# Kernel tuning notes

Hardware: AMD Instinct MI355X
Metric: run time of the kernel (lower is better)

## Reference

```python
import jax, jax.numpy as jnp
import numpy as np

H = 1024      # hidden_size
I = 512       # intermediate_size
E = 8         # n_routed_experts
TOPK = 2      # num_experts_per_tok
NGROUP = 4    # n_group
TOPKG = 2     # topk_group
SCALE = 1.0   # routed_scaling_factor
B, S = 4, 1024


def setup_inputs() -> dict:
    key = jax.random.key(0)
    k0, k1, k2, k3, k4 = jax.random.split(key, 5)
    return {
        "hidden_states": jax.random.normal(k0, (B, S, H), jnp.float32),
        "gate_weight": jax.random.normal(k1, (E, H), jnp.float32) * (1.0 / np.sqrt(H)),
        "e_score_correction_bias": jnp.zeros((E,), jnp.float32),
        "gate_proj": jax.random.normal(k2, (E, I, H), jnp.float32) * 0.02,
        "up_proj": jax.random.normal(k3, (E, I, H), jnp.float32) * 0.02,
        "down_proj": jax.random.normal(k4, (E, H, I), jnp.float32) * 0.02,
    }


def _gate(xf, gate_weight, bias):
    # xf: [T, H]
    T = xf.shape[0]
    logits = xf @ gate_weight.T                       # [T, E]
    scores = jax.nn.sigmoid(logits)
    scores_for_choice = scores + bias[None, :]
    gsz = E // NGROUP
    # group score: sum of top-2 corrected scores within each group
    grp = scores_for_choice.reshape(T, NGROUP, gsz)
    group_scores = jax.lax.top_k(grp, 2)[0].sum(-1)   # [T, NGROUP]
    _, group_idx = jax.lax.top_k(group_scores, TOPKG)  # [T, TOPKG]
    rows = jnp.arange(T)[:, None]
    group_mask = jnp.zeros((T, NGROUP), xf.dtype).at[rows, group_idx].set(1.0)
    score_mask = jnp.broadcast_to(group_mask[:, :, None], (T, NGROUP, gsz)).reshape(T, E)
    tmp_scores = jnp.where(score_mask > 0, scores_for_choice, 0.0)
    _, topk_idx = jax.lax.top_k(tmp_scores, TOPK)      # [T, TOPK]
    topk_weight = jnp.take_along_axis(scores, topk_idx, axis=1)
    if TOPK > 1:  # norm_topk_prob=True
        topk_weight = topk_weight / (topk_weight.sum(-1, keepdims=True) + 1e-20)
    topk_weight = topk_weight * SCALE
    return topk_idx, topk_weight


def reference(hidden_states, gate_weight, e_score_correction_bias,
              gate_proj, up_proj, down_proj):
    Bv, Sv, Hv = hidden_states.shape
    xf = hidden_states.reshape(-1, Hv).astype(jnp.float32)   # [T, H]
    topk_idx, topk_weight = _gate(xf, gate_weight.astype(jnp.float32),
                                  e_score_correction_bias.astype(jnp.float32))
    # Routed experts: loop over the small fixed expert set; each expert does a
    # dense GEMM over all tokens and results are combined with the (sparse)
    # per-token routing weight. Mathematically identical to the per-pair
    # gather-GEMM kernel, since expert output depends only on (token, expert).
    y = jnp.zeros_like(xf)
    for e in range(E):
        combine_w = jnp.where(topk_idx == e, topk_weight, 0.0).sum(-1)  # [T]
        g = xf @ gate_proj[e].T                                          # [T, I]
        u = xf @ up_proj[e].T                                            # [T, I]
        o = (jax.nn.silu(g) * u) @ down_proj[e].T                        # [T, H]
        y = y + combine_w[:, None] * o
    return y.reshape(Bv, Sv, Hv)
```

## Files before the change

kernel.cpp:

```cpp
#include <hip/hip_runtime.h>
#include <hip/hip_bf16.h>
#include <math.h>

#define H_DIM   1024
#define I_DIM   512
#define NEXP    8
#define NGROUP  4
#define T_TOK   4096
#define NPAIR   8192
#define SCALE   1.0f

typedef float f32x4 __attribute__((ext_vector_type(4)));
typedef short bf16x8 __attribute__((ext_vector_type(8)));
typedef short s16x4 __attribute__((ext_vector_type(4)));
typedef unsigned int u32;

static constexpr size_t OFF_ECNT  = 0;
static constexpr size_t OFF_ELIST = 1024;
static constexpr size_t OFF_EW    = OFF_ELIST + (size_t)NEXP * T_TOK * 4;
static constexpr size_t OFF_SEL   = 512 * 1024;
static constexpr size_t OFF_SELW  = 512 * 1024 + 64 * 1024;
static constexpr size_t MB = 1u << 20;
static constexpr size_t OFF_XH   = 1 * MB;
static constexpr size_t OFF_XL   = 9 * MB;
static constexpr size_t OFF_WGH  = 17 * MB;
static constexpr size_t OFF_WGL  = 25 * MB;
static constexpr size_t OFF_WUH  = 33 * MB;
static constexpr size_t OFF_WUL  = 41 * MB;
static constexpr size_t OFF_WDH  = 49 * MB;
static constexpr size_t OFF_WDL  = 57 * MB;
static constexpr size_t OFF_ACTH = 65 * MB;
static constexpr size_t OFF_ACTL = 73 * MB;
static constexpr size_t WS_NEED  = 81 * MB;
static constexpr size_t OFF_ACT_FB = 1 * MB;

__device__ __forceinline__ void gl_lds16(void* lds, const void* g) {
    __builtin_amdgcn_global_load_lds(
        (const __attribute__((address_space(1))) u32*)g,
        (__attribute__((address_space(3))) u32*)lds, 16, 0, 0);
}

__device__ __forceinline__ void split1(float v, short& h, short& l) {
    const u32 b = __float_as_uint(v);
    h = (short)(b >> 16);
    const float r = v - __uint_as_float(b & 0xffff0000u);
    l = (short)(__float_as_uint(r) >> 16);
}

__device__ __forceinline__ f32x4 mmac3(bf16x8 ah, bf16x8 al, bf16x8 bh,
                                       bf16x8 bl, f32x4 c) {
    c = __builtin_amdgcn_mfma_f32_16x16x32_bf16(ah, bh, c, 0, 0, 0);
    c = __builtin_amdgcn_mfma_f32_16x16x32_bf16(ah, bl, c, 0, 0, 0);
    c = __builtin_amdgcn_mfma_f32_16x16x32_bf16(al, bh, c, 0, 0, 0);
    return c;
}

__device__ __forceinline__ bf16x8 frag16(const short* tile, int row, int boff) {
    return *(const bf16x8*)((const char*)tile + row * 128 + boff);
}

__global__ __launch_bounds__(256)
void cvt_x_gate(const float* __restrict__ x,
                const float* __restrict__ gw,
                const float* __restrict__ bias,
                short* __restrict__ xh, short* __restrict__ xl,
                int* __restrict__ sel, float2* __restrict__ selw) {
    const int t = blockIdx.x;
    const int tid = threadIdx.x;
    const int lane = tid & 63;
    const int wv = tid >> 6;
    const int h = tid * 4;

    const f32x4 xv = *(const f32x4*)(x + (size_t)t * H_DIM + h);
    s16x4 hv, lv;
#pragma unroll
    for (int j = 0; j < 4; ++j) {
        short hh, ll;
        split1(xv[j], hh, ll);
        hv[j] = hh;
        lv[j] = ll;
    }
    *(s16x4*)(xh + (size_t)t * H_DIM + h) = hv;
    *(s16x4*)(xl + (size_t)t * H_DIM + h) = lv;

    float acc[NEXP];
#pragma unroll
    for (int e = 0; e < NEXP; ++e) {
        const f32x4 g = *(const f32x4*)(gw + e * H_DIM + h);
        float a = xv[0] * g[0];
        a = fmaf(xv[1], g[1], a);
        a = fmaf(xv[2], g[2], a);
        a = fmaf(xv[3], g[3], a);
        acc[e] = a;
    }
#pragma unroll
    for (int e = 0; e < NEXP; ++e) {
        float v = acc[e];
#pragma unroll
        for (int s = 32; s > 0; s >>= 1) v += __shfl_xor(v, s, 64);
        acc[e] = v;
    }
    __shared__ float red[4][NEXP];
    if (lane == 0) {
#pragma unroll
        for (int e = 0; e < NEXP; ++e) red[wv][e] = acc[e];
    }
    __syncthreads();
    if (tid == 0) {
        float scores[NEXP], corr[NEXP];
#pragma unroll
        for (int e = 0; e < NEXP; ++e) {
            const float s = red[0][e] + red[1][e] + red[2][e] + red[3][e];
            scores[e] = 1.0f / (1.0f + expf(-s));
            corr[e] = scores[e] + bias[e];
        }
        float gs[NGROUP];
#pragma unroll
        for (int g = 0; g < NGROUP; ++g) gs[g] = corr[2 * g] + corr[2 * g + 1];
        int g0 = 0;
#pragma unroll
        for (int g = 1; g < NGROUP; ++g) if (gs[g] > gs[g0]) g0 = g;
        int g1 = -1;
#pragma unroll
        for (int g = 0; g < NGROUP; ++g) {
            if (g == g0) continue;
            if (g1 < 0 || gs[g] > gs[g1]) g1 = g;
        }
        int e0 = -1;
#pragma unroll
        for (int e = 0; e < NEXP; ++e) {
            const int g = e >> 1;
            if (g != g0 && g != g1) continue;
            if (e0 < 0 || corr[e] > corr[e0]) e0 = e;
        }
        int e1 = -1;
#pragma unroll
        for (int e = 0; e < NEXP; ++e) {
            const int g = e >> 1;
            if ((g != g0 && g != g1) || e == e0) continue;
            if (e1 < 0 || corr[e] > corr[e1]) e1 = e;
        }
        float w0 = scores[e0], w1 = scores[e1];
        const float inv = 1.0f / (w0 + w1 + 1e-20f);
        w0 *= inv * SCALE;
        w1 *= inv * SCALE;
        sel[t] = e0 | (e1 << 8);
        selw[t] = make_float2(w0, w1);
    }
}

__global__ __launch_bounds__(256)
void build_lists(const int* __restrict__ sel, const float2* __restrict__ selw,
                 int* __restrict__ ecnt, int* __restrict__ elist,
                 float* __restrict__ elist_w) {
    const int e = blockIdx.x;
    const int tid = threadIdx.x;
    const int lane = tid & 63;
    const int wv = tid >> 6;
    const int base = tid * (T_TOK / 256);

    int c = 0;
#pragma unroll
    for (int i = 0; i < T_TOK / 256; ++i) {
        const int s = sel[base + i];
        if ((s & 0xff) == e || ((s >> 8) & 0xff) == e) ++c;
    }
    int v = c;
#pragma unroll
    for (int d = 1; d < 64; d <<= 1) {
        const int o = __shfl_up(v, d, 64);
        if (lane >= d) v += o;
    }
    __shared__ int wsum[4];
    if (lane == 63) wsum[wv] = v;
    __syncthreads();
    int waveoff = 0;
#pragma unroll
    for (int w = 0; w < 4; ++w) waveoff += (w < wv) ? wsum[w] : 0;
    int p = waveoff + v - c;
#pragma unroll
    for (int i = 0; i < T_TOK / 256; ++i) {
        const int t = base + i;
        const int s = sel[t];
        const float2 w2 = selw[t];
        if ((s & 0xff) == e) {
            elist[e * T_TOK + p] = t * 2;
            elist_w[e * T_TOK + p] = w2.x;
            ++p;
        } else if (((s >> 8) & 0xff) == e) {
            elist[e * T_TOK + p] = t * 2 + 1;
            elist_w[e * T_TOK + p] = w2.y;
            ++p;
        }
    }
    if (tid == 0) ecnt[e] = wsum[0] + wsum[1] + wsum[2] + wsum[3];
}

__global__ __launch_bounds__(256)
void cvt_w_kernel(const float* __restrict__ src, short* __restrict__ h,
                  short* __restrict__ l, int n) {
    const int i = (blockIdx.x * 256 + threadIdx.x) * 4;
    if (i >= n) return;
    const f32x4 v = *(const f32x4*)(src + i);
    s16x4 hv, lv;
#pragma unroll
    for (int j = 0; j < 4; ++j) {
        short hh, ll;
        split1(v[j], hh, ll);
        hv[j] = hh;
        lv[j] = ll;
    }
    *(s16x4*)(h + i) = hv;
    *(s16x4*)(l + i) = lv;
}

__global__ __launch_bounds__(256)
void gemm1_planar(const short* __restrict__ xh, const short* __restrict__ xl,
                  const short* __restrict__ wgh, const short* __restrict__ wgl,
                  const short* __restrict__ wuh, const short* __restrict__ wul,
                  const int* __restrict__ ecnt, const int* __restrict__ elist,
                  short* __restrict__ acth, short* __restrict__ actl) {
    const int e = blockIdx.z;
    const int cnt = ecnt[e];
    const int row0 = blockIdx.x * 64;
    if (row0 >= cnt) return;
    const int col0 = blockIdx.y * 64;

    __shared__ __align__(16) short xhb[4096], xlb[4096];
    __shared__ __align__(16) short ghb[4096], glb[4096];
    __shared__ __align__(16) short uhb[4096], ulb[4096];

    const int tid = threadIdx.x, lane = tid & 63, wv = tid >> 6;
    const int wr = wv >> 1, wc = wv & 1;
    const int laneR = lane & 15, laneQ = lane >> 4;
    const int* el = elist + e * T_TOK;

    size_t xoff[2], woff[2];
    int ldso[2];
#pragma unroll
    for (int l = 0; l < 2; ++l) {
        const int ci = tid + l * 256;
        const int row = ci >> 3;
        const int c = (ci & 7) ^ (row & 7);
        ldso[l] = ci * 16;
        const int rr = row0 + row;
        const int v = (rr < cnt) ? el[rr] : 0;
        xoff[l] = (size_t)(v >> 1) * H_DIM + c * 8;
        woff[l] = ((size_t)e * I_DIM + col0 + row) * H_DIM + c * 8;
    }

    f32x4 ag[2][2], au[2][2];
#pragma unroll
    for (int m = 0; m < 2; ++m)
#pragma unroll
        for (int n = 0; n < 2; ++n) { ag[m][n] = (f32x4)0.0f; au[m][n] = (f32x4)0.0f; }

    for (int k0 = 0; k0 < H_DIM; k0 += 64) {
        __syncthreads();
#pragma unroll
        for (int l = 0; l < 2; ++l) {
            gl_lds16((char*)xhb + ldso[l], xh + xoff[l] + k0);
            gl_lds16((char*)xlb + ldso[l], xl + xoff[l] + k0);
            gl_lds16((char*)ghb + ldso[l], wgh + woff[l] + k0);
            gl_lds16((char*)glb + ldso[l], wgl + woff[l] + k0);
            gl_lds16((char*)uhb + ldso[l], wuh + woff[l] + k0);
            gl_lds16((char*)ulb + ldso[l], wul + woff[l] + k0);
        }
        __syncthreads();

#pragma unroll
        for (int ks = 0; ks < 2; ++ks) {
            const int boff = (ks * 64 + laneQ * 16) ^ ((laneR & 7) << 4);
            bf16x8 xh_[2], xl_[2];
#pragma unroll
            for (int m = 0; m < 2; ++m) {
                const int r = wr * 32 + m * 16 + laneR;
                xh_[m] = frag16(xhb, r, boff);
                xl_[m] = frag16(xlb, r, boff);
            }
            bf16x8 gh_[2], gl_[2], uh_[2], ul_[2];
#pragma unroll
            for (int n = 0; n < 2; ++n) {
                const int r = wc * 32 + n * 16 + laneR;
                gh_[n] = frag16(ghb, r, boff);
                gl_[n] = frag16(glb, r, boff);
                uh_[n] = frag16(uhb, r, boff);
                ul_[n] = frag16(ulb, r, boff);
            }
#pragma unroll
            for (int m = 0; m < 2; ++m)
#pragma unroll
                for (int n = 0; n < 2; ++n) {
                    ag[m][n] = mmac3(xh_[m], xl_[m], gh_[n], gl_[n], ag[m][n]);
                    au[m][n] = mmac3(xh_[m], xl_[m], uh_[n], ul_[n], au[m][n]);
                }
        }
    }

#pragma unroll
    for (int m = 0; m < 2; ++m) {
        const int rl = wr * 32 + m * 16 + laneQ * 4;
#pragma unroll
        for (int j = 0; j < 4; ++j) {
            const int rr = row0 + rl + j;
            if (rr >= cnt) continue;
            const int v = el[rr];
#pragma unroll
            for (int n = 0; n < 2; ++n) {
                const int col = col0 + wc * 32 + n * 16 + laneR;
                const float g = ag[m][n][j];
                const float u = au[m][n][j];
                const float val = (g / (1.0f + __expf(-g))) * u;
                short hh, ll;
                split1(val, hh, ll);
                acth[(size_t)v * I_DIM + col] = hh;
                actl[(size_t)v * I_DIM + col] = ll;
            }
        }
    }
}

__global__ __launch_bounds__(256)
void gemm2_planar(const short* __restrict__ acth, const short* __restrict__ actl,
                  const short* __restrict__ wdh, const short* __restrict__ wdl,
                  const int* __restrict__ ecnt, const int* __restrict__ elist,
                  const float* __restrict__ elist_w, float* __restrict__ out) {
    const int e = blockIdx.z;
    const int cnt = ecnt[e];
    const int row0 = blockIdx.x * 64;
    if (row0 >= cnt) return;
    const int col0 = blockIdx.y * 64;

    __shared__ __align__(16) short ahb[4096], alb[4096];
    __shared__ __align__(16) short dhb[4096], dlb[4096];

    const int tid = threadIdx.x, lane = tid & 63, wv = tid >> 6;
    const int wr = wv >> 1, wc = wv & 1;
    const int laneR = lane & 15, laneQ = lane >> 4;
    const int* el = elist + e * T_TOK;
    const float* elw = elist_w + e * T_TOK;

    size_t aoff[2], woff[2];
    int ldso[2];
#pragma unroll
    for (int l = 0; l < 2; ++l) {
        const int ci = tid + l * 256;
        const int row = ci >> 3;
        const int c = (ci & 7) ^ (row & 7);
        ldso[l] = ci * 16;
        const int rr = row0 + row;
        const int v = (rr < cnt) ? el[rr] : 0;
        aoff[l] = (size_t)v * I_DIM + c * 8;
        woff[l] = ((size_t)e * H_DIM + col0 + row) * I_DIM + c * 8;
    }

    f32x4 acc[2][2];
#pragma unroll
    for (int m = 0; m < 2; ++m)
#pragma unroll
        for (int n = 0; n < 2; ++n) acc[m][n] = (f32x4)0.0f;

    for (int k0 = 0; k0 < I_DIM; k0 += 64) {
        __syncthreads();
#pragma unroll
        for (int l = 0; l < 2; ++l) {
            gl_lds16((char*)ahb + ldso[l], acth + aoff[l] + k0);
            gl_lds16((char*)alb + ldso[l], actl + aoff[l] + k0);
            gl_lds16((char*)dhb + ldso[l], wdh + woff[l] + k0);
            gl_lds16((char*)dlb + ldso[l], wdl + woff[l] + k0);
        }
        __syncthreads();

#pragma unroll
        for (int ks = 0; ks < 2; ++ks) {
            const int boff = (ks * 64 + laneQ * 16) ^ ((laneR & 7) << 4);
            bf16x8 ah_[2], al_[2];
#pragma unroll
            for (int m = 0; m < 2; ++m) {
                const int r = wr * 32 + m * 16 + laneR;
                ah_[m] = frag16(ahb, r, boff);
                al_[m] = frag16(alb, r, boff);
            }
            bf16x8 bh_[2], bl_[2];
#pragma unroll
            for (int n = 0; n < 2; ++n) {
                const int r = wc * 32 + n * 16 + laneR;
                bh_[n] = frag16(dhb, r, boff);
                bl_[n] = frag16(dlb, r, boff);
            }
#pragma unroll
            for (int m = 0; m < 2; ++m)
#pragma unroll
                for (int n = 0; n < 2; ++n)
                    acc[m][n] = mmac3(ah_[m], al_[m], bh_[n], bl_[n], acc[m][n]);
        }
    }

#pragma unroll
    for (int m = 0; m < 2; ++m) {
        const int rl = wr * 32 + m * 16 + laneQ * 4;
#pragma unroll
        for (int j = 0; j < 4; ++j) {
            const int rr = row0 + rl + j;
            if (rr >= cnt) continue;
            const int v = el[rr];
            const float w = elw[rr];
            float* orow = out + (size_t)(v >> 1) * H_DIM;
#pragma unroll
            for (int n = 0; n < 2; ++n) {
                const int col = col0 + wc * 32 + n * 16 + laneR;
                atomicAdd(&orow[col], w * acc[m][n][j]);
            }
        }
    }
}

__device__ __forceinline__ void cvt8(const f32x4& a, const f32x4& b,
                                     bf16x8& hi, bf16x8& lo) {
#pragma unroll
    for (int j = 0; j < 4; ++j) {
        short hh, ll;
        split1(a[j], hh, ll);
        ((short*)&hi)[j] = hh;
        ((short*)&lo)[j] = ll;
    }
#pragma unroll
    for (int j = 0; j < 4; ++j) {
        short hh, ll;
        split1(b[j], hh, ll);
        ((short*)&hi)[4 + j] = hh;
        ((short*)&lo)[4 + j] = ll;
    }
}

__device__ __forceinline__ void frag_ld(const float* tile, int row, int off1,
                                        bf16x8& hi, bf16x8& lo) {
    const char* p = (const char*)tile + row * 256;
    const f32x4 a = *(const f32x4*)(p + off1);
    const f32x4 b = *(const f32x4*)(p + (off1 ^ 16));
    cvt8(a, b, hi, lo);
}

__global__ __launch_bounds__(256)
void gate_kernel(const float* __restrict__ x, const float* __restrict__ gw,
                 const float* __restrict__ bias, int* __restrict__ ecnt,
                 int* __restrict__ elist, float* __restrict__ elist_w) {
    const int wave = threadIdx.x >> 6;
    const int lane = threadIdx.x & 63;
    const int t = blockIdx.x * 4 + wave;
    if (t >= T_TOK) return;
    const float* xr = x + (size_t)t * H_DIM;
    float acc[NEXP];
#pragma unroll
    for (int e = 0; e < NEXP; ++e) acc[e] = 0.0f;
    for (int h = lane; h < H_DIM; h += 64) {
        const float xv = xr[h];
#pragma unroll
        for (int e = 0; e < NEXP; ++e) acc[e] = fmaf(xv, gw[e * H_DIM + h], acc[e]);
    }
#pragma unroll
    for (int e = 0; e < NEXP; ++e) {
        float v = acc[e];
#pragma unroll
        for (int s = 32; s > 0; s >>= 1) v += __shfl_xor(v, s, 64);
        acc[e] = v;
    }
    if (lane == 0) {
        float scores[NEXP], corr[NEXP];
#pragma unroll
        for (int e = 0; e < NEXP; ++e) {
            scores[e] = 1.0f / (1.0f + expf(-acc[e]));
            corr[e] = scores[e] + bias[e];
        }
        float gs[NGROUP];
#pragma unroll
        for (int g = 0; g < NGROUP; ++g) gs[g] = corr[2 * g] + corr[2 * g + 1];
        int g0 = 0;
#pragma unroll
        for (int g = 1; g < NGROUP; ++g) if (gs[g] > gs[g0]) g0 = g;
        int g1 = -1;
#pragma unroll
        for (int g = 0; g < NGROUP; ++g) {
            if (g == g0) continue;
            if (g1 < 0 || gs[g] > gs[g1]) g1 = g;
        }
        int e0 = -1;
#pragma unroll
        for (int e = 0; e < NEXP; ++e) {
            const int g = e >> 1;
            if (g != g0 && g != g1) continue;
            if (e0 < 0 || corr[e] > corr[e0]) e0 = e;
        }
        int e1 = -1;
#pragma unroll
        for (int e = 0; e < NEXP; ++e) {
            const int g = e >> 1;
            if ((g != g0 && g != g1) || e == e0) continue;
            if (e1 < 0 || corr[e] > corr[e1]) e1 = e;
        }
        float w0 = scores[e0], w1 = scores[e1];
        const float inv = 1.0f / (w0 + w1 + 1e-20f);
        w0 *= inv * SCALE;
        w1 *= inv * SCALE;
        const int p0 = atomicAdd(&ecnt[e0], 1);
        elist[e0 * T_TOK + p0] = t * 2 + 0;
        elist_w[e0 * T_TOK + p0] = w0;
        const int p1 = atomicAdd(&ecnt[e1], 1);
        elist[e1 * T_TOK + p1] = t * 2 + 1;
        elist_w[e1 * T_TOK + p1] = w1;
    }
}

__global__ __launch_bounds__(256)
void gemm1_fb(const float* __restrict__ x, const float* __restrict__ wg_all,
              const float* __restrict__ wu_all, const int* __restrict__ ecnt,
              const int* __restrict__ elist, float* __restrict__ act) {
    const int e = blockIdx.z;
    const int cnt = ecnt[e];
    const int row0 = blockIdx.x * 64;
    if (row0 >= cnt) return;
    const int col0 = blockIdx.y * 64;
    __shared__ __align__(16) float xs[64 * 64], gsm[64 * 64], usm[64 * 64];
    const int tid = threadIdx.x, lane = tid & 63, wv = tid >> 6;
    const int wr = wv >> 1, wc = wv & 1;
    const int laneR = lane & 15, laneQ = lane >> 4;
    const int* el = elist + e * T_TOK;
    const float* xrow[4]; const float* grow[4]; const float* urow[4];
    int coff[4], ldso[4];
#pragma unroll
    for (int l = 0; l < 4; ++l) {
        const int ci = tid + l * 256;
        const int row = ci >> 4;
        const int c = (ci & 15) ^ (row & 15);
        coff[l] = c * 4; ldso[l] = ci * 16;
        const int rr = row0 + row;
        const int v = (rr < cnt) ? el[rr] : 0;
        xrow[l] = x + (size_t)(v >> 1) * H_DIM;
        grow[l] = wg_all + (size_t)e * I_DIM * H_DIM + (size_t)(col0 + row) * H_DIM;
        urow[l] = wu_all + (size_t)e * I_DIM * H_DIM + (size_t)(col0 + row) * H_DIM;
    }
    f32x4 ag[2][2], au[2][2];
#pragma unroll
    for (int m = 0; m < 2; ++m)
#pragma unroll
        for (int n = 0; n < 2; ++n) { ag[m][n] = (f32x4)0.0f; au[m][n] = (f32x4)0.0f; }
    for (int k0 = 0; k0 < H_DIM; k0 += 64) {
        __syncthreads();
#pragma unroll
        for (int l = 0; l < 4; ++l) {
            gl_lds16((char*)xs + ldso[l], xrow[l] + k0 + coff[l]);
            gl_lds16((char*)gsm + ldso[l], grow[l] + k0 + coff[l]);
            gl_lds16((char*)usm + ldso[l], urow[l] + k0 + coff[l]);
        }
        __syncthreads();
#pragma unroll
        for (int ks = 0; ks < 2; ++ks) {
            const int off1 = ((ks * 128 + laneQ * 32) ^ (laneR << 4));
            bf16x8 xh[2], xl[2];
#pragma unroll
            for (int m = 0; m < 2; ++m)
                frag_ld(xs, wr * 32 + m * 16 + laneR, off1, xh[m], xl[m]);
            bf16x8 gh[2], gl[2], uh[2], ul[2];
#pragma unroll
            for (int n = 0; n < 2; ++n) {
                frag_ld(gsm, wc * 32 + n * 16 + laneR, off1, gh[n], gl[n]);
                frag_ld(usm, wc * 32 + n * 16 + laneR, off1, uh[n], ul[n]);
            }
#pragma unroll
            for (int m = 0; m < 2; ++m)
#pragma unroll
                for (int n = 0; n < 2; ++n) {
                    ag[m][n] = mmac3(xh[m], xl[m], gh[n], gl[n], ag[m][n]);
                    au[m][n] = mmac3(xh[m], xl[m], uh[n], ul[n], au[m][n]);
                }
        }
    }
#pragma unroll
    for (int m = 0; m < 2; ++m) {
        const int rl = wr * 32 + m * 16 + laneQ * 4;
#pragma unroll
        for (int j = 0; j < 4; ++j) {
            const int rr = row0 + rl + j;
            if (rr >= cnt) continue;
            const int v = el[rr];
            float* arow = act + (size_t)v * I_DIM;
#pragma unroll
            for (int n = 0; n < 2; ++n) {
                const int col = col0 + wc * 32 + n * 16 + laneR;
                const float g = ag[m][n][j];
                const float u = au[m][n][j];
                arow[col] = (g / (1.0f + __expf(-g))) * u;
            }
        }
    }
}

__global__ __launch_bounds__(256)
void gemm2_fb(const float* __restrict__ act, const float* __restrict__ wd_all,
              const int* __restrict__ ecnt, const int* __restrict__ elist,
              const float* __restrict__ elist_w, float* __restrict__ out) {
    const int e = blockIdx.z;
    const int cnt = ecnt[e];
    const int row0 = blockIdx.x * 64;
    if (row0 >= cnt) return;
    const int col0 = blockIdx.y * 64;
    __shared__ __align__(16) float as[64 * 64], dsm[64 * 64];
    const int tid = threadIdx.x, lane = tid & 63, wv = tid >> 6;
    const int wr = wv >> 1, wc = wv & 1;
    const int laneR = lane & 15, laneQ = lane >> 4;
    const int* el = elist + e * T_TOK;
    const float* elw = elist_w + e * T_TOK;
    const float* arow[4]; const float* drow[4];
    int coff[4], ldso[4];
#pragma unroll
    for (int l = 0; l < 4; ++l) {
        const int ci = tid + l * 256;
        const int row = ci >> 4;
        const int c = (ci & 15) ^ (row & 15);
        coff[l] = c * 4; ldso[l] = ci * 16;
        const int rr = row0 + row;
        const int v = (rr < cnt) ? el[rr] : 0;
        arow[l] = act + (size_t)v * I_DIM;
        drow[l] = wd_all + (size_t)e * H_DIM * I_DIM + (size_t)(col0 + row) * I_DIM;
    }
    f32x4 acc[2][2];
#pragma unroll
    for (int m = 0; m < 2; ++m)
#pragma unroll
        for (int n = 0; n < 2; ++n) acc[m][n] = (f32x4)0.0f;
    for (int k0 = 0; k0 < I_DIM; k0 += 64) {
        __syncthreads();
#pragma unroll
        for (int l = 0; l < 4; ++l) {
            gl_lds16((char*)as + ldso[l], arow[l] + k0 + coff[l]);
            gl_lds16((char*)dsm + ldso[l], drow[l] + k0 + coff[l]);
        }
        __syncthreads();
#pragma unroll
        for (int ks = 0; ks < 2; ++ks) {
            const int off1 = ((ks * 128 + laneQ * 32) ^ (laneR << 4));
            bf16x8 ah[2], al[2];
#pragma unroll
            for (int m = 0; m < 2; ++m)
                frag_ld(as, wr * 32 + m * 16 + laneR, off1, ah[m], al[m]);
            bf16x8 bh[2], bl[2];
#pragma unroll
            for (int n = 0; n < 2; ++n)
                frag_ld(dsm, wc * 32 + n * 16 + laneR, off1, bh[n], bl[n]);
#pragma unroll
            for (int m = 0; m < 2; ++m)
#pragma unroll
                for (int n = 0; n < 2; ++n)
                    acc[m][n] = mmac3(ah[m], al[m], bh[n], bl[n], acc[m][n]);
        }
    }
#pragma unroll
    for (int m = 0; m < 2; ++m) {
        const int rl = wr * 32 + m * 16 + laneQ * 4;
#pragma unroll
        for (int j = 0; j < 4; ++j) {
            const int rr = row0 + rl + j;
            if (rr >= cnt) continue;
            const int v = el[rr];
            const float w = elw[rr];
            float* orow = out + (size_t)(v >> 1) * H_DIM;
#pragma unroll
            for (int n = 0; n < 2; ++n) {
                const int col = col0 + wc * 32 + n * 16 + laneR;
                atomicAdd(&orow[col], w * acc[m][n][j]);
            }
        }
    }
}

extern "C" void kernel_launch(void* const* d_in, const int* in_sizes, int n_in,
                              void* d_out, int out_size, void* d_ws, size_t ws_size,
                              hipStream_t stream) {
    const float* x    = (const float*)d_in[0];
    const float* gw   = (const float*)d_in[1];
    const float* bias = (const float*)d_in[2];
    const float* wg   = (const float*)d_in[3];
    const float* wu   = (const float*)d_in[4];
    const float* wd   = (const float*)d_in[5];
    float* out = (float*)d_out;

    char* ws = (char*)d_ws;
    int*   ecnt    = (int*)(ws + OFF_ECNT);
    int*   elist   = (int*)(ws + OFF_ELIST);
    float* elist_w = (float*)(ws + OFF_EW);

    (void)hipMemsetAsync(ecnt, 0, 64, stream);
    (void)hipMemsetAsync(out, 0, (size_t)out_size * sizeof(float), stream);

    if (ws_size >= WS_NEED) {
        int*    sel  = (int*)(ws + OFF_SEL);
        float2* selw = (float2*)(ws + OFF_SELW);
        short* xh   = (short*)(ws + OFF_XH);
        short* xl   = (short*)(ws + OFF_XL);
        short* wgh  = (short*)(ws + OFF_WGH);
        short* wgl  = (short*)(ws + OFF_WGL);
        short* wuh  = (short*)(ws + OFF_WUH);
        short* wul  = (short*)(ws + OFF_WUL);
        short* wdh  = (short*)(ws + OFF_WDH);
        short* wdl  = (short*)(ws + OFF_WDL);
        short* acth = (short*)(ws + OFF_ACTH);
        short* actl = (short*)(ws + OFF_ACTL);

        const int nW = NEXP * I_DIM * H_DIM;
        cvt_w_kernel<<<nW / 1024, 256, 0, stream>>>(wg, wgh, wgl, nW);
        cvt_w_kernel<<<nW / 1024, 256, 0, stream>>>(wu, wuh, wul, nW);
        cvt_w_kernel<<<nW / 1024, 256, 0, stream>>>(wd, wdh, wdl, nW);
        cvt_x_gate<<<T_TOK, 256, 0, stream>>>(x, gw, bias, xh, xl, sel, selw);
        build_lists<<<NEXP, 256, 0, stream>>>(sel, selw, ecnt, elist, elist_w);
        gemm1_planar<<<dim3(T_TOK / 64, I_DIM / 64, NEXP), 256, 0, stream>>>(
            xh, xl, wgh, wgl, wuh, wul, ecnt, elist, acth, actl);
        gemm2_planar<<<dim3(T_TOK / 64, H_DIM / 64, NEXP), 256, 0, stream>>>(
            acth, actl, wdh, wdl, ecnt, elist, elist_w, out);
    } else {
        float* act = (float*)(ws + OFF_ACT_FB);
        gate_kernel<<<T_TOK / 4, 256, 0, stream>>>(x, gw, bias, ecnt, elist, elist_w);
        gemm1_fb<<<dim3(T_TOK / 64, I_DIM / 64, NEXP), 256, 0, stream>>>(
            x, wg, wu, ecnt, elist, act);
        gemm2_fb<<<dim3(T_TOK / 64, H_DIM / 64, NEXP), 256, 0, stream>>>(
            act, wd, ecnt, elist, elist_w, out);
    }
}
```

Before: 299.5 us.

## Double-buffer LDS tiles and enlarge expert GEMM blocks to 128 rows

Both expert GEMM kernels now use 512-thread blocks covering 128 token rows by 64 columns. Shared-memory tiles are double-buffered so the next K-slice is loaded while the current one is multiplied, with one barrier per iteration instead of two. The larger row tile shares each weight tile across twice as many tokens, cutting weight traffic. The cost is doubled LDS per block (about 96 KB for gemm1), which may lower occupancy, and more partly empty tiles for experts with few tokens.

```diff
diff --git a/kernel.cpp b/kernel.cpp
--- a/kernel.cpp
+++ b/kernel.cpp
@@ -214,40 +214,42 @@
     *(s16x4*)(l + i) = lv;
 }
 
-__global__ __launch_bounds__(256)
-void gemm1_planar(const short* __restrict__ xh, const short* __restrict__ xl,
-                  const short* __restrict__ wgh, const short* __restrict__ wgl,
-                  const short* __restrict__ wuh, const short* __restrict__ wul,
-                  const int* __restrict__ ecnt, const int* __restrict__ elist,
-                  short* __restrict__ acth, short* __restrict__ actl) {
+__global__ __launch_bounds__(512)
+void gemm1_p2(const short* __restrict__ xh, const short* __restrict__ xl,
+              const short* __restrict__ wgh, const short* __restrict__ wgl,
+              const short* __restrict__ wuh, const short* __restrict__ wul,
+              const int* __restrict__ ecnt, const int* __restrict__ elist,
+              short* __restrict__ acth, short* __restrict__ actl) {
     const int e = blockIdx.z;
     const int cnt = ecnt[e];
-    const int row0 = blockIdx.x * 64;
+    const int row0 = blockIdx.x * 128;
     if (row0 >= cnt) return;
     const int col0 = blockIdx.y * 64;
 
-    __shared__ __align__(16) short xhb[4096], xlb[4096];
-    __shared__ __align__(16) short ghb[4096], glb[4096];
-    __shared__ __align__(16) short uhb[4096], ulb[4096];
+    __shared__ __align__(16) short xhb[2][8192], xlb[2][8192];
+    __shared__ __align__(16) short ghb[2][4096], glb[2][4096];
+    __shared__ __align__(16) short uhb[2][4096], ulb[2][4096];
 
     const int tid = threadIdx.x, lane = tid & 63, wv = tid >> 6;
     const int wr = wv >> 1, wc = wv & 1;
     const int laneR = lane & 15, laneQ = lane >> 4;
     const int* el = elist + e * T_TOK;
 
-    size_t xoff[2], woff[2];
-    int ldso[2];
+    size_t xoff[2]; int xls[2];
 #pragma unroll
     for (int l = 0; l < 2; ++l) {
-        const int ci = tid + l * 256;
+        const int ci = tid + l * 512;
         const int row = ci >> 3;
         const int c = (ci & 7) ^ (row & 7);
-        ldso[l] = ci * 16;
+        xls[l] = ci * 16;
         const int rr = row0 + row;
         const int v = (rr < cnt) ? el[rr] : 0;
         xoff[l] = (size_t)(v >> 1) * H_DIM + c * 8;
-        woff[l] = ((size_t)e * I_DIM + col0 + row) * H_DIM + c * 8;
-    }
+    }
+    const int wrow = tid >> 3;
+    const int wcc = (tid & 7) ^ (wrow & 7);
+    const size_t woff = ((size_t)e * I_DIM + col0 + wrow) * H_DIM + wcc * 8;
+    const int wls = tid * 16;
 
     f32x4 ag[2][2], au[2][2];
 #pragma unroll
@@ -255,19 +257,28 @@
 #pragma unroll
         for (int n = 0; n < 2; ++n) { ag[m][n] = (f32x4)0.0f; au[m][n] = (f32x4)0.0f; }
 
+#define STAGE1(B, K0)                                         \
+    do {                                                      \
+        gl_lds16((char*)xhb[B] + xls[0], xh + xoff[0] + (K0));\
+        gl_lds16((char*)xhb[B] + xls[1], xh + xoff[1] + (K0));\
+        gl_lds16((char*)xlb[B] + xls[0], xl + xoff[0] + (K0));\
+        gl_lds16((char*)xlb[B] + xls[1], xl + xoff[1] + (K0));\
+        gl_lds16((char*)ghb[B] + wls, wgh + woff + (K0));     \
+        gl_lds16((char*)glb[B] + wls, wgl + woff + (K0));     \
+        gl_lds16((char*)uhb[B] + wls, wuh + woff + (K0));     \
+        gl_lds16((char*)ulb[B] + wls, wul + woff + (K0));     \
+    } while (0)
+
+    STAGE1(0, 0);
+    __syncthreads();
+    int cur = 0;
     for (int k0 = 0; k0 < H_DIM; k0 += 64) {
-        __syncthreads();
-#pragma unroll
-        for (int l = 0; l < 2; ++l) {
-            gl_lds16((char*)xhb + ldso[l], xh + xoff[l] + k0);
-            gl_lds16((char*)xlb + ldso[l], xl + xoff[l] + k0);
-            gl_lds16((char*)ghb + ldso[l], wgh + woff[l] + k0);
-            gl_lds16((char*)glb + ldso[l], wgl + woff[l] + k0);
-            gl_lds16((char*)uhb + ldso[l], wuh + woff[l] + k0);
-            gl_lds16((char*)ulb + ldso[l], wul + woff[l] + k0);
-        }
-        __syncthreads();
-
+        if (k0 + 64 < H_DIM) {
+            if (cur) STAGE1(0, k0 + 64); else STAGE1(1, k0 + 64);
+        }
+        const short* xhT = xhb[cur]; const short* xlT = xlb[cur];
+        const short* ghT = ghb[cur]; const short* glT = glb[cur];
+        const short* uhT = uhb[cur]; const short* ulT = ulb[cur];
 #pragma unroll
         for (int ks = 0; ks < 2; ++ks) {
             const int boff = (ks * 64 + laneQ * 16) ^ ((laneR & 7) << 4);
@@ -275,17 +286,17 @@
 #pragma unroll
             for (int m = 0; m < 2; ++m) {
                 const int r = wr * 32 + m * 16 + laneR;
-                xh_[m] = frag16(xhb, r, boff);
-                xl_[m] = frag16(xlb, r, boff);
+                xh_[m] = frag16(xhT, r, boff);
+                xl_[m] = frag16(xlT, r, boff);
             }
             bf16x8 gh_[2], gl_[2], uh_[2], ul_[2];
 #pragma unroll
             for (int n = 0; n < 2; ++n) {
                 const int r = wc * 32 + n * 16 + laneR;
-                gh_[n] = frag16(ghb, r, boff);
-                gl_[n] = frag16(glb, r, boff);
-                uh_[n] = frag16(uhb, r, boff);
-                ul_[n] = frag16(ulb, r, boff);
+                gh_[n] = frag16(ghT, r, boff);
+                gl_[n] = frag16(glT, r, boff);
+                uh_[n] = frag16(uhT, r, boff);
+                ul_[n] = frag16(ulT, r, boff);
             }
 #pragma unroll
             for (int m = 0; m < 2; ++m)
@@ -295,7 +306,10 @@
                     au[m][n] = mmac3(xh_[m], xl_[m], uh_[n], ul_[n], au[m][n]);
                 }
         }
-    }
+        __syncthreads();
+        cur ^= 1;
+    }
+#undef STAGE1
 
 #pragma unroll
     for (int m = 0; m < 2; ++m) {
@@ -320,19 +334,19 @@
     }
 }
 
-__global__ __launch_bounds__(256)
-void gemm2_planar(const short* __restrict__ acth, const short* __restrict__ actl,
-                  const short* __restrict__ wdh, const short* __restrict__ wdl,
-                  const int* __restrict__ ecnt, const int* __restrict__ elist,
-                  const float* __restrict__ elist_w, float* __restrict__ out) {
+__global__ __launch_bounds__(512)
+void gemm2_p2(const short* __restrict__ acth, const short* __restrict__ actl,
+              const short* __restrict__ wdh, const short* __restrict__ wdl,
+              const int* __restrict__ ecnt, const int* __restrict__ elist,
+              const float* __restrict__ elist_w, float* __restrict__ out) {
     const int e = blockIdx.z;
     const int cnt = ecnt[e];
-    const int row0 = blockIdx.x * 64;
+    const int row0 = blockIdx.x * 128;
     if (row0 >= cnt) return;
     const int col0 = blockIdx.y * 64;
 
-    __shared__ __align__(16) short ahb[4096], alb[4096];
-    __shared__ __align__(16) short dhb[4096], dlb[4096];
+    __shared__ __align__(16) short ahb[2][8192], alb[2][8192];
+    __shared__ __align__(16) short dhb[2][4096], dlb[2][4096];
 
     const int tid = threadIdx.x, lane = tid & 63, wv = tid >> 6;
     const int wr = wv >> 1, wc = wv & 1;
@@ -340,19 +354,21 @@
     const int* el = elist + e * T_TOK;
     const float* elw = elist_w + e * T_TOK;
 
-    size_t aoff[2], woff[2];
-    int ldso[2];
+    size_t aoff[2]; int als[2];
 #pragma unroll
     for (int l = 0; l < 2; ++l) {
-        const int ci = tid + l * 256;
+        const int ci = tid + l * 512;
         const int row = ci >> 3;
         const int c = (ci & 7) ^ (row & 7);
-        ldso[l] = ci * 16;
+        als[l] = ci * 16;
         const int rr = row0 + row;
         const int v = (rr < cnt) ? el[rr] : 0;
         aoff[l] = (size_t)v * I_DIM + c * 8;
-        woff[l] = ((size_t)e * H_DIM + col0 + row) * I_DIM + c * 8;
-    }
+    }
+    const int wrow = tid >> 3;
+    const int wcc = (tid & 7) ^ (wrow & 7);
+    const size_t woff = ((size_t)e * H_DIM + col0 + wrow) * I_DIM + wcc * 8;
+    const int wls = tid * 16;
 
     f32x4 acc[2][2];
 #pragma unroll
@@ -360,17 +376,25 @@
 #pragma unroll
         for (int n = 0; n < 2; ++n) acc[m][n] = (f32x4)0.0f;
 
+#define STAGE2(B, K0)                                            \
+    do {                                                         \
+        gl_lds16((char*)ahb[B] + als[0], acth + aoff[0] + (K0)); \
+        gl_lds16((char*)ahb[B] + als[1], acth + aoff[1] + (K0)); \
+        gl_lds16((char*)alb[B] + als[0], actl + aoff[0] + (K0)); \
+        gl_lds16((char*)alb[B] + als[1], actl + aoff[1] + (K0)); \
+        gl_lds16((char*)dhb[B] + wls, wdh + woff + (K0));        \
+        gl_lds16((char*)dlb[B] + wls, wdl + woff + (K0));        \
+    } while (0)
+
+    STAGE2(0, 0);
+    __syncthreads();
+    int cur = 0;
     for (int k0 = 0; k0 < I_DIM; k0 += 64) {
-        __syncthreads();
-#pragma unroll
-        for (int l = 0; l < 2; ++l) {
-            gl_lds16((char*)ahb + ldso[l], acth + aoff[l] + k0);
-            gl_lds16((char*)alb + ldso[l], actl + aoff[l] + k0);
-            gl_lds16((char*)dhb + ldso[l], wdh + woff[l] + k0);
-            gl_lds16((char*)dlb + ldso[l], wdl + woff[l] + k0);
-        }
-        __syncthreads();
-
+        if (k0 + 64 < I_DIM) {
+            if (cur) STAGE2(0, k0 + 64); else STAGE2(1, k0 + 64);
+        }
+        const short* ahT = ahb[cur]; const short* alT = alb[cur];
+        const short* dhT = dhb[cur]; const short* dlT = dlb[cur];
 #pragma unroll
         for (int ks = 0; ks < 2; ++ks) {
             const int boff = (ks * 64 + laneQ * 16) ^ ((laneR & 7) << 4);
@@ -378,15 +402,15 @@
 #pragma unroll
             for (int m = 0; m < 2; ++m) {
                 const int r = wr * 32 + m * 16 + laneR;
-                ah_[m] = frag16(ahb, r, boff);
-                al_[m] = frag16(alb, r, boff);
+                ah_[m] = frag16(ahT, r, boff);
+                al_[m] = frag16(alT, r, boff);
             }
             bf16x8 bh_[2], bl_[2];
 #pragma unroll
             for (int n = 0; n < 2; ++n) {
                 const int r = wc * 32 + n * 16 + laneR;
-                bh_[n] = frag16(dhb, r, boff);
-                bl_[n] = frag16(dlb, r, boff);
+                bh_[n] = frag16(dhT, r, boff);
+                bl_[n] = frag16(dlT, r, boff);
             }
 #pragma unroll
             for (int m = 0; m < 2; ++m)
@@ -394,7 +418,10 @@
                 for (int n = 0; n < 2; ++n)
                     acc[m][n] = mmac3(ah_[m], al_[m], bh_[n], bl_[n], acc[m][n]);
         }
-    }
+        __syncthreads();
+        cur ^= 1;
+    }
+#undef STAGE2
 
 #pragma unroll
     for (int m = 0; m < 2; ++m) {
@@ -712,9 +739,9 @@
         cvt_w_kernel<<<nW / 1024, 256, 0, stream>>>(wd, wdh, wdl, nW);
         cvt_x_gate<<<T_TOK, 256, 0, stream>>>(x, gw, bias, xh, xl, sel, selw);
         build_lists<<<NEXP, 256, 0, stream>>>(sel, selw, ecnt, elist, elist_w);
-        gemm1_planar<<<dim3(T_TOK / 64, I_DIM / 64, NEXP), 256, 0, stream>>>(
+        gemm1_p2<<<dim3(T_TOK / 128, I_DIM / 64, NEXP), 512, 0, stream>>>(
             xh, xl, wgh, wgl, wuh, wul, ecnt, elist, acth, actl);
-        gemm2_planar<<<dim3(T_TOK / 64, H_DIM / 64, NEXP), 256, 0, stream>>>(
+        gemm2_p2<<<dim3(T_TOK / 128, H_DIM / 64, NEXP), 512, 0, stream>>>(
             acth, actl, wdh, wdl, ecnt, elist, elist_w, out);
     } else {
         float* act = (float*)(ws + OFF_ACT_FB);
```

Measured after the change: 526.4 us. 1.76x slower.
